# Kernel tuning notes

Hardware: AMD Instinct MI355X
Metric: run time of the kernel (lower is better)

## Reference

```python
import jax, jax.numpy as jnp
import numpy as np

N = 100000      # nodes
E = 1600000     # edges (avg degree 16)
F_IN = 10       # float features; x also carries 2 int index columns
H = 128         # hidden_dim
G = 1000        # graphs
GAP = 3         # gap_len
NPG = N // G    # nodes per graph


def _lin(k, i, o):
    # xavier-uniform-ish init
    lim = np.sqrt(6.0 / (i + o)).astype(np.float32)
    return jax.random.uniform(k, (i, o), jnp.float32, -lim, lim)


def setup_inputs() -> dict:
    key = jax.random.key(0)
    ks = jax.random.split(key, 32)
    xf = jax.random.normal(ks[0], (N, F_IN), jnp.float32)
    ship = jax.random.randint(ks[1], (N, 1), 0, 10).astype(jnp.float32)
    nav = jax.random.randint(ks[2], (N, 1), 0, 10).astype(jnp.float32)
    x = jnp.concatenate([xf, ship, nav], axis=1)  # [N, F_IN+2]
    edge_index = jax.random.randint(ks[3], (2, E), 0, N)
    batch = jnp.arange(N, dtype=jnp.int32) // NPG  # sorted graph ids
    d_in = F_IN + 8  # strip 2 idx cols, add two 4-dim embeddings
    inp = dict(
        x=x, edge_index=edge_index, batch=batch,
        ship_emb=jax.random.normal(ks[4], (10, 4), jnp.float32),
        nav_emb=jax.random.normal(ks[5], (10, 4), jnp.float32),
        W1=_lin(ks[6], d_in, H), b1=jnp.zeros((H,), jnp.float32),
        W2=_lin(ks[7], H, H), b2=jnp.zeros((H,), jnp.float32),
        W3=_lin(ks[8], H, H), b3=jnp.zeros((H,), jnp.float32),
        # GRU params, stored pre-transposed: x @ Wih, gate order (r,z,n)
        Wih_f=_lin(ks[9], H, 3 * H), Whh_f=_lin(ks[10], H, 3 * H),
        bih_f=jnp.zeros((3 * H,), jnp.float32), bhh_f=jnp.zeros((3 * H,), jnp.float32),
        Wih_b=_lin(ks[11], H, 3 * H), Whh_b=_lin(ks[12], H, 3 * H),
        bih_b=jnp.zeros((3 * H,), jnp.float32), bhh_b=jnp.zeros((3 * H,), jnp.float32),
        Wred=_lin(ks[13], 2 * H, H), bred=jnp.zeros((H,), jnp.float32),
        Wh1=_lin(ks[14], 2 * H, H), bh1=jnp.zeros((H,), jnp.float32),
        Wh2=_lin(ks[15], H, 2), bh2=jnp.zeros((2,), jnp.float32),
        num_graphs=G, gap_start_idx=4,
    )
    return inp


def _gru_cell(x, h, Wih, Whh, bih, bhh):
    gi = x @ Wih + bih
    gh = h @ Whh + bhh
    ir, iz, in_ = jnp.split(gi, 3, axis=-1)
    hr, hz, hn = jnp.split(gh, 3, axis=-1)
    r = jax.nn.sigmoid(ir + hr)
    z = jax.nn.sigmoid(iz + hz)
    n = jnp.tanh(in_ + r * hn)
    return (1.0 - z) * n + z * h


def reference(x, edge_index, batch, ship_emb, nav_emb,
              W1, b1, W2, b2, W3, b3,
              Wih_f, Whh_f, bih_f, bhh_f, Wih_b, Whh_b, bih_b, bhh_b,
              Wred, bred, Wh1, bh1, Wh2, bh2, num_graphs, gap_start_idx):
    n_nodes = x.shape[0]
    st = x[:, -2].astype(jnp.int32)
    nv = x[:, -1].astype(jnp.int32)
    feats = jnp.concatenate([x[:, :-2], ship_emb[st], nav_emb[nv]], axis=1)

    src, dst = edge_index[0], edge_index[1]
    # GCN symmetric norm with self-loops: deg over targets + 1
    deg = jax.ops.segment_sum(jnp.ones_like(dst, jnp.float32), dst, num_segments=n_nodes) + 1.0
    dis = jax.lax.rsqrt(deg)  # deg^{-1/2}
    norm = (dis[src] * dis[dst])[:, None]
    self_norm = (dis * dis)[:, None]

    def gcn(h, W, b):
        m = h @ W  # [N,H]
        agg = jax.ops.segment_sum(m[src] * norm, dst, num_segments=n_nodes)
        return agg + m * self_norm + b

    # dropout is eval-mode identity
    h = jax.nn.relu(gcn(feats, W1, b1))
    h = jax.nn.relu(gcn(h, W2, b2))
    h = jax.nn.relu(gcn(h, W3, b3))

    # per-graph gap node = graph offset + gap_start_idx
    counts = jax.ops.segment_sum(jnp.ones_like(batch, jnp.float32), batch, num_segments=num_graphs)
    offsets = jnp.concatenate([jnp.zeros((1,), jnp.float32), jnp.cumsum(counts)[:-1]]).astype(jnp.int32)
    h0 = h[offsets + gap_start_idx]  # [G,H]

    inp, hf, hb = h0, h0, h0
    preds = []
    for _ in range(GAP):
        hf = _gru_cell(inp, hf, Wih_f, Whh_f, bih_f, bhh_f)
        hb = _gru_cell(inp, hb, Wih_b, Whh_b, bih_b, bhh_b)
        out = jnp.concatenate([hf, hb], axis=-1)  # [G,2H]
        preds.append(jax.nn.relu(out @ Wh1 + bh1) @ Wh2 + bh2)
        inp = out @ Wred + bred
    return jnp.stack(preds, axis=1)  # [G, gap_len, 2]
```

## Files before the change

### kernel.cpp

```cpp
#include <hip/hip_runtime.h>
#include <math.h>

#define H 128
#define GAPLEN 3
#define DIN 18

static inline int ceil_div(int a, int b){ return (a + b - 1) / b; }

__device__ __forceinline__ unsigned int bf16pk2(float a, float b){
  unsigned int ua = __float_as_uint(a);
  ua = (ua + 0x7fffu + ((ua >> 16) & 1u)) >> 16;
  unsigned int ub = __float_as_uint(b);
  ub = (ub + 0x7fffu + ((ub >> 16) & 1u)) >> 16;
  return ua | (ub << 16);
}
__device__ __forceinline__ float bf16lo(unsigned int u){ return __uint_as_float(u << 16); }
__device__ __forceinline__ float bf16hi(unsigned int u){ return __uint_as_float(u & 0xffff0000u); }

#define CHUNK 4096

__global__ __launch_bounds__(256) void bhistA_k(const int* __restrict__ ei, int* __restrict__ bh,
                                                int E, int NB){
  __shared__ int lh[1024];
  int t = threadIdx.x;
  for (int j = t; j < 1024; j += 256) lh[j] = 0;
  __syncthreads();
  int base = blockIdx.x * CHUNK;
#pragma unroll
  for (int i = 0; i < 16; ++i){
    int e = base + i * 256 + t;
    if (e < E) atomicAdd(&lh[ei[E + e] >> 7], 1);
  }
  __syncthreads();
  for (int j = t; j < NB; j += 256){
    int v = lh[j];
    if (v) atomicAdd(&bh[j], v);
  }
}

__global__ void bscan_k(const int* __restrict__ bh, int* __restrict__ bbase, int NB){
  __shared__ int sd[1024];
  int t = threadIdx.x;
  int v = (t < NB) ? bh[t] : 0;
  sd[t] = v;
  __syncthreads();
  for (int off = 1; off < 1024; off <<= 1){
    int add = (t >= off) ? sd[t - off] : 0;
    __syncthreads();
    sd[t] += add;
    __syncthreads();
  }
  if (t < NB) bbase[t] = sd[t] - v;
}

__global__ __launch_bounds__(256) void bpartC_k(const int* __restrict__ ei,
                                                const int* __restrict__ bbase,
                                                int* __restrict__ bcur,
                                                int* __restrict__ ebuf, int E, int NB){
  __shared__ int lh[1024];
  __shared__ int lchunk[1024];
  __shared__ int lcur[1024];
  int t = threadIdx.x;
  for (int j = t; j < 1024; j += 256) lh[j] = 0;
  __syncthreads();
  int base = blockIdx.x * CHUNK;
  int pk[16], bk[16];
#pragma unroll
  for (int i = 0; i < 16; ++i){
    int e = base + i * 256 + t;
    if (e < E){
      int s = ei[e];
      int d = ei[E + e];
      bk[i] = d >> 7;
      pk[i] = ((d & 127) << 17) | s;
      atomicAdd(&lh[bk[i]], 1);
    } else bk[i] = -1;
  }
  __syncthreads();
  for (int j = t; j < NB; j += 256){
    int c = lh[j];
    if (c) lchunk[j] = bbase[j] + atomicAdd(&bcur[j], c);
    lcur[j] = 0;
  }
  __syncthreads();
#pragma unroll
  for (int i = 0; i < 16; ++i){
    if (bk[i] >= 0){
      int off = atomicAdd(&lcur[bk[i]], 1);
      ebuf[lchunk[bk[i]] + off] = pk[i];
    }
  }
}

__global__ __launch_bounds__(256) void bbuildD_k(const int* __restrict__ ebuf,
                                                 const int* __restrict__ bh,
                                                 const int* __restrict__ bbase,
                                                 int* __restrict__ rp, int* __restrict__ cnt,
                                                 float* __restrict__ dis, int* __restrict__ csr,
                                                 int n){
  __shared__ int hist[128], sc[128], gb[128], curr[128];
  int b = blockIdx.x;
  int t = threadIdx.x;
  int sb = bbase[b];
  int mb = bh[b];
  if (t < 128) hist[t] = 0;
  __syncthreads();
  for (int i = t; i < mb; i += 256)
    atomicAdd(&hist[ebuf[sb + i] >> 17], 1);
  __syncthreads();
  if (t < 128) sc[t] = hist[t];
  __syncthreads();
  for (int off = 1; off < 128; off <<= 1){
    int add = (t < 128 && t >= off) ? sc[t - off] : 0;
    __syncthreads();
    if (t < 128) sc[t] += add;
    __syncthreads();
  }
  if (t < 128){
    int node = b * 128 + t;
    int rpv = sb + sc[t] - hist[t];
    gb[t] = rpv;
    curr[t] = 0;
    if (node < n){
      rp[node] = rpv;
      cnt[node] = hist[t];
      dis[node] = rsqrtf((float)hist[t] + 1.0f);
    }
  }
  __syncthreads();
  for (int i = t; i < mb; i += 256){
    int p = ebuf[sb + i];
    int dl = p >> 17;
    int src = p & 0x1FFFF;
    int off = atomicAdd(&curr[dl], 1);
    csr[gb[dl] + off] = src;
  }
}

__global__ void dhist_k(const int* __restrict__ cnt, int* __restrict__ dh, int n){
  __shared__ int lh[256];
  int t = threadIdx.x;
  lh[t] = 0;
  __syncthreads();
  int i = blockIdx.x * 256 + t;
  if (i < n){
    int d = cnt[i]; if (d > 255) d = 255;
    atomicAdd(&lh[d], 1);
  }
  __syncthreads();
  if (lh[t]) atomicAdd(&dh[t], lh[t]);
}

__global__ void dscan_k(const int* __restrict__ dh, int* __restrict__ dbase){
  __shared__ int sd[256];
  int t = threadIdx.x;
  int v = dh[t];
  sd[t] = v;
  __syncthreads();
  for (int off = 1; off < 256; off <<= 1){
    int add = (t >= off) ? sd[t - off] : 0;
    __syncthreads();
    sd[t] += add;
    __syncthreads();
  }
  dbase[t] = sd[t] - v;
}

__global__ void dperm_k(const int* __restrict__ cnt, const int* __restrict__ rp,
                        const float* __restrict__ dis, const int* __restrict__ dbase,
                        int* __restrict__ dcur, int4* __restrict__ prc, int n){
  __shared__ int lh[256], lbase[256], lcur[256];
  int t = threadIdx.x;
  lh[t] = 0;
  __syncthreads();
  int i = blockIdx.x * 256 + t;
  bool ok = i < n;
  int d = 0, db = 0;
  if (ok){
    d = cnt[i]; db = d > 255 ? 255 : d;
    atomicAdd(&lh[db], 1);
  }
  __syncthreads();
  int c = lh[t];
  lcur[t] = 0;
  if (c) lbase[t] = dbase[t] + atomicAdd(&dcur[t], c);
  __syncthreads();
  if (ok){
    int off = atomicAdd(&lcur[db], 1);
    int pos = lbase[db] + off;
    prc[pos] = int4{rp[i], d, i, __float_as_int(dis[i])};
  }
}

__global__ void build_feats_k(const float* __restrict__ x, const float* __restrict__ se,
                              const float* __restrict__ ne, const float* __restrict__ dis,
                              unsigned int* __restrict__ f16, int n){
  int i = blockIdx.x * 256 + threadIdx.x;
  if (i >= n) return;
  const float* xr = x + (size_t)i * 12;
  float di = dis[i];
  float v[18];
#pragma unroll
  for (int c = 0; c < 10; ++c) v[c] = di * xr[c];
  int st = (int)xr[10];
  int nv = (int)xr[11];
#pragma unroll
  for (int c = 0; c < 4; ++c){
    v[10 + c] = di * se[st * 4 + c];
    v[14 + c] = di * ne[nv * 4 + c];
  }
  unsigned int* fr = f16 + (size_t)i * 9;
#pragma unroll
  for (int q = 0; q < 9; ++q) fr[q] = bf16pk2(v[2*q], v[2*q + 1]);
}

__global__ __launch_bounds__(256) void agg18b_k(const unsigned int* __restrict__ fw16,
                                                const int4* __restrict__ prc,
                                                const int* __restrict__ csr,
                                                float* __restrict__ out, int n){
  int i = blockIdx.x * 16 + (threadIdx.x >> 4);
  if (i >= n) return;
  int4 v = prc[i];
  int start = v.x, m = v.y, node = v.z;
  float di = __int_as_float(v.w);
  int lane = threadIdx.x & 15;
  bool act = lane < 9;
  float ax = 0.f, ay = 0.f, bx = 0.f, by = 0.f;
  int e = 0;
  for (; e + 4 <= m; e += 4){
    int s0 = csr[start + e + 0];
    int s1 = csr[start + e + 1];
    int s2 = csr[start + e + 2];
    int s3 = csr[start + e + 3];
    if (act){
      unsigned int u0 = fw16[(size_t)s0 * 9 + lane];
      unsigned int u1 = fw16[(size_t)s1 * 9 + lane];
      unsigned int u2 = fw16[(size_t)s2 * 9 + lane];
      unsigned int u3 = fw16[(size_t)s3 * 9 + lane];
      ax += bf16lo(u0) + bf16lo(u1);  ay += bf16hi(u0) + bf16hi(u1);
      bx += bf16lo(u2) + bf16lo(u3);  by += bf16hi(u2) + bf16hi(u3);
    }
  }
  for (; e < m; ++e){
    int s = csr[start + e];
    if (act){
      unsigned int u = fw16[(size_t)s * 9 + lane];
      ax += bf16lo(u); ay += bf16hi(u);
    }
  }
  if (act){
    unsigned int su = fw16[(size_t)node * 9 + lane];
    float2 o;
    o.x = di * (ax + bx + bf16lo(su));
    o.y = di * (ay + by + bf16hi(su));
    *(float2*)&out[(size_t)node * DIN + lane * 2] = o;
  }
}

__global__ __launch_bounds__(256) void agg128b_k(const unsigned int* __restrict__ hw16,
                                                 const int4* __restrict__ prc,
                                                 const int* __restrict__ csr,
                                                 float* __restrict__ out, int n){
  int i = blockIdx.x * 4 + (threadIdx.x >> 6);
  if (i >= n) return;
  int4 v = prc[i];
  int start = __builtin_amdgcn_readfirstlane(v.x);
  int m     = __builtin_amdgcn_readfirstlane(v.y);
  int node  = __builtin_amdgcn_readfirstlane(v.z);
  float di  = __int_as_float(__builtin_amdgcn_readfirstlane(v.w));
  int l = threadIdx.x & 63;
  const unsigned int* hp = hw16 + l;
  float ax0 = 0.f, ay0 = 0.f, ax1 = 0.f, ay1 = 0.f;
  float ax2 = 0.f, ay2 = 0.f, ax3 = 0.f, ay3 = 0.f;
  int e = 0;
  for (; e + 8 <= m; e += 8){
    int s0 = csr[start + e + 0];
    int s1 = csr[start + e + 1];
    int s2 = csr[start + e + 2];
    int s3 = csr[start + e + 3];
    int s4 = csr[start + e + 4];
    int s5 = csr[start + e + 5];
    int s6 = csr[start + e + 6];
    int s7 = csr[start + e + 7];
    unsigned int u0 = hp[(size_t)s0 << 6];
    unsigned int u1 = hp[(size_t)s1 << 6];
    unsigned int u2 = hp[(size_t)s2 << 6];
    unsigned int u3 = hp[(size_t)s3 << 6];
    unsigned int u4 = hp[(size_t)s4 << 6];
    unsigned int u5 = hp[(size_t)s5 << 6];
    unsigned int u6 = hp[(size_t)s6 << 6];
    unsigned int u7 = hp[(size_t)s7 << 6];
    ax0 += bf16lo(u0) + bf16lo(u1);  ay0 += bf16hi(u0) + bf16hi(u1);
    ax1 += bf16lo(u2) + bf16lo(u3);  ay1 += bf16hi(u2) + bf16hi(u3);
    ax2 += bf16lo(u4) + bf16lo(u5);  ay2 += bf16hi(u4) + bf16hi(u5);
    ax3 += bf16lo(u6) + bf16lo(u7);  ay3 += bf16hi(u6) + bf16hi(u7);
  }
  for (; e < m; ++e){
    int s = csr[start + e];
    unsigned int u = hp[(size_t)s << 6];
    ax0 += bf16lo(u); ay0 += bf16hi(u);
  }
  unsigned int su = hp[(size_t)node << 6];
  float2 o;
  o.x = di * (ax0 + ax1 + ax2 + ax3 + bf16lo(su));
  o.y = di * (ay0 + ay1 + ay2 + ay3 + bf16hi(su));
  ((float2*)out)[(size_t)node * 64 + l] = o;
}

__global__ void gemm18_k(const float* __restrict__ A, const float* __restrict__ W,
                         const float* __restrict__ b, const float* __restrict__ dis,
                         unsigned int* __restrict__ C16, int n){
  __shared__ float sw[DIN * H];
  __shared__ float sb[H];
  __shared__ float sa[8][DIN];
  int t = threadIdx.x;
  for (int i = t; i < DIN * H; i += 256) sw[i] = W[i];
  if (t < H) sb[t] = b[t];
  int row0 = blockIdx.x * 8;
  for (int i = t; i < 8 * DIN; i += 256){
    int r = i / DIN, c = i % DIN;
    int rr = row0 + r;
    sa[r][c] = (rr < n) ? A[(size_t)rr * DIN + c] : 0.f;
  }
  __syncthreads();
  int r = t >> 5, lane = t & 31;
  int row = row0 + r;
  if (row >= n) return;
  int c0 = lane * 4;
  float ox = sb[c0], oy = sb[c0 + 1], oz = sb[c0 + 2], ow = sb[c0 + 3];
#pragma unroll
  for (int k = 0; k < DIN; ++k){
    float a = sa[r][k];
    const float4 w = *(const float4*)&sw[k * H + c0];
    ox += a * w.x; oy += a * w.y; oz += a * w.z; ow += a * w.w;
  }
  float di = dis[row];
  uint2 pk;
  pk.x = bf16pk2(di * fmaxf(ox, 0.f), di * fmaxf(oy, 0.f));
  pk.y = bf16pk2(di * fmaxf(oz, 0.f), di * fmaxf(ow, 0.f));
  *(uint2*)&C16[(size_t)row * 64 + lane * 2] = pk;
}

template<int OUTMODE>
__global__ __launch_bounds__(128) void gemm128_k(const float* __restrict__ A,
                                                 const float* __restrict__ B,
                                                 const float* __restrict__ bias,
                                                 const float* __restrict__ dis,
                                                 float* __restrict__ C,
                                                 unsigned int* __restrict__ C16, int n){
  __shared__ float sa[32][64];
  int t = threadIdx.x;
  int row0 = blockIdx.x * 64;
  int tc = t & 15;
  int tr = t >> 4;
  float acc[8][8];
#pragma unroll
  for (int i = 0; i < 8; ++i)
#pragma unroll
    for (int j = 0; j < 8; ++j) acc[i][j] = 0.f;

  int lr = t >> 1;
  int lc = (t & 1) * 16;
  for (int k0 = 0; k0 < H; k0 += 32){
    const float* Ar = A + (size_t)(row0 + lr) * H + k0 + lc;
    bool rowok = (row0 + lr) < n;
    float4 v0, v1, v2, v3;
    if (rowok){
      v0 = *(const float4*)(Ar + 0);
      v1 = *(const float4*)(Ar + 4);
      v2 = *(const float4*)(Ar + 8);
      v3 = *(const float4*)(Ar + 12);
    } else {
      v0 = v1 = v2 = v3 = float4{0.f, 0.f, 0.f, 0.f};
    }
    __syncthreads();
    float vv[16] = {v0.x, v0.y, v0.z, v0.w, v1.x, v1.y, v1.z, v1.w,
                    v2.x, v2.y, v2.z, v2.w, v3.x, v3.y, v3.z, v3.w};
#pragma unroll
    for (int i = 0; i < 16; ++i) sa[lc + i][lr] = vv[i];
    __syncthreads();

    const float* Bp = B + (size_t)k0 * H + tc * 8;
#pragma unroll
    for (int k = 0; k < 32; ++k){
      float4 b0 = *(const float4*)(Bp + (size_t)k * H);
      float4 b1 = *(const float4*)(Bp + (size_t)k * H + 4);
      float4 a0 = *(const float4*)&sa[k][tr * 8];
      float4 a1 = *(const float4*)&sa[k][tr * 8 + 4];
      float aa[8] = {a0.x, a0.y, a0.z, a0.w, a1.x, a1.y, a1.z, a1.w};
      float bb[8] = {b0.x, b0.y, b0.z, b0.w, b1.x, b1.y, b1.z, b1.w};
#pragma unroll
      for (int i = 0; i < 8; ++i)
#pragma unroll
        for (int j = 0; j < 8; ++j) acc[i][j] += aa[i] * bb[j];
    }
  }
  float bb[8];
#pragma unroll
  for (int j = 0; j < 8; ++j) bb[j] = bias[tc * 8 + j];
#pragma unroll
  for (int i = 0; i < 8; ++i){
    int row = row0 + tr * 8 + i;
    if (row < n){
      float o0 = fmaxf(acc[i][0] + bb[0], 0.f);
      float o1 = fmaxf(acc[i][1] + bb[1], 0.f);
      float o2 = fmaxf(acc[i][2] + bb[2], 0.f);
      float o3 = fmaxf(acc[i][3] + bb[3], 0.f);
      float o4 = fmaxf(acc[i][4] + bb[4], 0.f);
      float o5 = fmaxf(acc[i][5] + bb[5], 0.f);
      float o6 = fmaxf(acc[i][6] + bb[6], 0.f);
      float o7 = fmaxf(acc[i][7] + bb[7], 0.f);
      if (OUTMODE == 0){
        float di = dis[row];
        uint4 pk;
        pk.x = bf16pk2(di * o0, di * o1);
        pk.y = bf16pk2(di * o2, di * o3);
        pk.z = bf16pk2(di * o4, di * o5);
        pk.w = bf16pk2(di * o6, di * o7);
        *(uint4*)&C16[(size_t)row * 64 + tc * 4] = pk;
      } else {
        float* Cp = C + (size_t)row * H + tc * 8;
        *(float4*)(Cp)     = float4{o0, o1, o2, o3};
        *(float4*)(Cp + 4) = float4{o4, o5, o6, o7};
      }
    }
  }
}

__global__ void ghist_k(const int* __restrict__ batch, int* __restrict__ gc, int n){
  int i = blockIdx.x * 256 + threadIdx.x;
  if (i < n) atomicAdd(&gc[batch[i]], 1);
}

__global__ void gscan_k(const int* __restrict__ gc, int* __restrict__ go, int G){
  __shared__ int sd[1024];
  int t = threadIdx.x;
  int v = (t < G) ? gc[t] : 0;
  sd[t] = v;
  __syncthreads();
  for (int off = 1; off < 1024; off <<= 1){
    int add = (t >= off) ? sd[t - off] : 0;
    __syncthreads();
    sd[t] += add;
    __syncthreads();
  }
  if (t < G) go[t] = sd[t] - v;
}

__global__ void gather_k(const float* __restrict__ h3, const int* __restrict__ go,
                         const int* __restrict__ gap,
                         float* __restrict__ inp, float* __restrict__ hf,
                         float* __restrict__ hb, int G){
  int g = blockIdx.x;
  int t = threadIdx.x;
  if (g >= G) return;
  int idx = go[g] + gap[0];
  float v = h3[(size_t)idx * H + t];
  inp[(size_t)g * H + t] = v;
  hf[(size_t)g * H + t] = v;
  hb[(size_t)g * H + t] = v;
}

#define GPB 4
__device__ __forceinline__ float sigf(float x){ return 1.f / (1.f + expf(-x)); }

__global__ __launch_bounds__(256) void gru_step_k(
    const float* __restrict__ inp, float* __restrict__ hf, float* __restrict__ hb,
    const float* __restrict__ Wih_f, const float* __restrict__ Whh_f,
    const float* __restrict__ bih_f, const float* __restrict__ bhh_f,
    const float* __restrict__ Wih_b, const float* __restrict__ Whh_b,
    const float* __restrict__ bih_b, const float* __restrict__ bhh_b, int G){
  int cell = blockIdx.y;
  const float* Wih = cell ? Wih_b : Wih_f;
  const float* Whh = cell ? Whh_b : Whh_f;
  const float* bih = cell ? bih_b : bih_f;
  const float* bhh = cell ? bhh_b : bhh_f;
  float* h = cell ? hb : hf;

  __shared__ float sx[GPB][H];
  __shared__ float sh[GPB][H];
  int g0 = blockIdx.x * GPB;
  int t = threadIdx.x;
  for (int i = t; i < GPB * H; i += 256){
    int g = i >> 7, c = i & 127;
    int gg = g0 + g;
    sx[g][c] = (gg < G) ? inp[(size_t)gg * H + c] : 0.f;
    sh[g][c] = (gg < G) ? h[(size_t)gg * H + c] : 0.f;
  }
  __syncthreads();
  int j = t & 127;
  int gs = (t >> 7) * 2;
  float ir[2] = {0,0}, iz[2] = {0,0}, in_[2] = {0,0};
  float hr[2] = {0,0}, hz[2] = {0,0}, hn[2] = {0,0};
#pragma unroll 4
  for (int k = 0; k < H; ++k){
    const float* wi = Wih + (size_t)k * 384;
    const float* wh = Whh + (size_t)k * 384;
    float wr = wi[j], wz = wi[128 + j], wn = wi[256 + j];
    float ur = wh[j], uz = wh[128 + j], un = wh[256 + j];
#pragma unroll
    for (int g = 0; g < 2; ++g){
      float xv = sx[gs + g][k];
      float hv = sh[gs + g][k];
      ir[g] += xv * wr; iz[g] += xv * wz; in_[g] += xv * wn;
      hr[g] += hv * ur; hz[g] += hv * uz; hn[g] += hv * un;
    }
  }
  float bir = bih[j], biz = bih[128 + j], bin = bih[256 + j];
  float bhr = bhh[j], bhz = bhh[128 + j], bhn = bhh[256 + j];
#pragma unroll
  for (int g = 0; g < 2; ++g){
    int gg = g0 + gs + g;
    if (gg < G){
      float r = sigf(ir[g] + bir + hr[g] + bhr);
      float z = sigf(iz[g] + biz + hz[g] + bhz);
      float nn = tanhf(in_[g] + bin + r * (hn[g] + bhn));
      float hv = sh[gs + g][j];
      h[(size_t)gg * H + j] = (1.f - z) * nn + z * hv;
    }
  }
}

__global__ __launch_bounds__(256) void post_step_k(
    const float* __restrict__ hf, const float* __restrict__ hb,
    const float* __restrict__ Wred, const float* __restrict__ bred,
    const float* __restrict__ Wh1, const float* __restrict__ bh1,
    const float* __restrict__ Wh2, const float* __restrict__ bh2,
    float* __restrict__ inp, float* __restrict__ out, int G, int tstep){
  __shared__ float so[GPB][256];
  __shared__ float st1[GPB][H];
  int g0 = blockIdx.x * GPB;
  int t = threadIdx.x;
  for (int i = t; i < GPB * H; i += 256){
    int g = i >> 7, c = i & 127;
    int gg = g0 + g;
    so[g][c]       = (gg < G) ? hf[(size_t)gg * H + c] : 0.f;
    so[g][128 + c] = (gg < G) ? hb[(size_t)gg * H + c] : 0.f;
  }
  __syncthreads();
  int j = t & 127;
  int gs = (t >> 7) * 2;
  float a1[2] = {0,0}, a2[2] = {0,0};
#pragma unroll 8
  for (int k = 0; k < 256; ++k){
    float w1 = Wh1[(size_t)k * H + j];
    float w2 = Wred[(size_t)k * H + j];
#pragma unroll
    for (int g = 0; g < 2; ++g){
      float o = so[gs + g][k];
      a1[g] += o * w1;
      a2[g] += o * w2;
    }
  }
  float B1 = bh1[j], BR = bred[j];
#pragma unroll
  for (int g = 0; g < 2; ++g){
    int gg = g0 + gs + g;
    float t1 = fmaxf(a1[g] + B1, 0.f);
    st1[gs + g][j] = (gg < G) ? t1 : 0.f;
    if (gg < G) inp[(size_t)gg * H + j] = a2[g] + BR;
  }
  __syncthreads();
  if (t < GPB * 2){
    int g = t >> 1, o = t & 1;
    int gg = g0 + g;
    if (gg < G){
      float s = bh2[o];
#pragma unroll 8
      for (int k = 0; k < H; ++k) s += st1[g][k] * Wh2[k * 2 + o];
      out[((size_t)gg * GAPLEN + tstep) * 2 + o] = s;
    }
  }
}

extern "C" void kernel_launch(void* const* d_in, const int* in_sizes, int n_in,
                              void* d_out, int out_size, void* d_ws, size_t ws_size,
                              hipStream_t stream) {
  const float* x     = (const float*)d_in[0];
  const int*   ei    = (const int*)d_in[1];
  const int*   batch = (const int*)d_in[2];
  const float* semb  = (const float*)d_in[3];
  const float* nemb  = (const float*)d_in[4];
  const float* W1 = (const float*)d_in[5];  const float* b1 = (const float*)d_in[6];
  const float* W2 = (const float*)d_in[7];  const float* b2 = (const float*)d_in[8];
  const float* W3 = (const float*)d_in[9];  const float* b3 = (const float*)d_in[10];
  const float* Wih_f = (const float*)d_in[11]; const float* Whh_f = (const float*)d_in[12];
  const float* bih_f = (const float*)d_in[13]; const float* bhh_f = (const float*)d_in[14];
  const float* Wih_b = (const float*)d_in[15]; const float* Whh_b = (const float*)d_in[16];
  const float* bih_b = (const float*)d_in[17]; const float* bhh_b = (const float*)d_in[18];
  const float* Wred = (const float*)d_in[19]; const float* bred = (const float*)d_in[20];
  const float* Wh1  = (const float*)d_in[21]; const float* bh1  = (const float*)d_in[22];
  const float* Wh2  = (const float*)d_in[23]; const float* bh2  = (const float*)d_in[24];
  const int* gap = (const int*)d_in[26];

  int N = in_sizes[0] / 12;
  int E = in_sizes[1] / 2;
  int G = out_size / (GAPLEN * 2);
  int NB = ceil_div(N, 128);
  float* out = (float*)d_out;

  char* ws = (char*)d_ws;
  size_t off = 0;
  auto alloc = [&](size_t bytes) -> void* {
    void* p = ws + off;
    off += (bytes + 511) & ~(size_t)511;
    return p;
  };
  unsigned int* feats16 = (unsigned int*)alloc((size_t)N * 9 * 4);
  float* agg1   = (float*)alloc((size_t)N * DIN * 4);
  float* bufA   = (float*)alloc((size_t)N * H * 4);
  float* bufB   = (float*)alloc((size_t)N * H * 4);
  unsigned int* hb16 = (unsigned int*)alloc((size_t)N * H * 2);
  int*   cnt    = (int*)alloc((size_t)N * 4);
  float* dis    = (float*)alloc((size_t)N * 4);
  int*   rp     = (int*)alloc((size_t)N * 4);
  int*   csr    = (int*)alloc((size_t)E * 4);
  int*   ebuf   = (int*)alloc((size_t)E * 4);
  int4*  prc    = (int4*)alloc((size_t)N * 16);
  int*   bh     = (int*)alloc((size_t)NB * 4);
  int*   bbase  = (int*)alloc((size_t)NB * 4);
  int*   bcur   = (int*)alloc((size_t)NB * 4);
  int*   dh     = (int*)alloc(256 * 4);
  int*   dbase  = (int*)alloc(256 * 4);
  int*   dcur   = (int*)alloc(256 * 4);
  int*   gc     = (int*)alloc((size_t)G * 4);
  int*   go     = (int*)alloc((size_t)G * 4);
  float* ginp   = (float*)alloc((size_t)G * H * 4);
  float* ghf    = (float*)alloc((size_t)G * H * 4);
  float* ghb    = (float*)alloc((size_t)G * H * 4);
  (void)ws_size; (void)n_in;

  hipMemsetAsync(bh, 0, (size_t)NB * 4, stream);
  hipMemsetAsync(bcur, 0, (size_t)NB * 4, stream);
  hipMemsetAsync(dh, 0, 256 * 4, stream);
  hipMemsetAsync(dcur, 0, 256 * 4, stream);
  hipMemsetAsync(gc, 0, (size_t)G * 4, stream);

  int nb256 = ceil_div(N, 256);
  int ebC   = ceil_div(E, CHUNK);

  bhistA_k<<<ebC, 256, 0, stream>>>(ei, bh, E, NB);
  bscan_k<<<1, 1024, 0, stream>>>(bh, bbase, NB);
  bpartC_k<<<ebC, 256, 0, stream>>>(ei, bbase, bcur, ebuf, E, NB);
  bbuildD_k<<<NB, 256, 0, stream>>>(ebuf, bh, bbase, rp, cnt, dis, csr, N);
  dhist_k<<<nb256, 256, 0, stream>>>(cnt, dh, N);
  dscan_k<<<1, 256, 0, stream>>>(dh, dbase);
  dperm_k<<<nb256, 256, 0, stream>>>(cnt, rp, dis, dbase, dcur, prc, N);
  build_feats_k<<<nb256, 256, 0, stream>>>(x, semb, nemb, dis, feats16, N);

  int gemmb = ceil_div(N, 64);

  agg18b_k<<<ceil_div(N, 16), 256, 0, stream>>>(feats16, prc, csr, agg1, N);
  gemm18_k<<<ceil_div(N, 8), 256, 0, stream>>>(agg1, W1, b1, dis, hb16, N);
  agg128b_k<<<ceil_div(N, 4), 256, 0, stream>>>(hb16, prc, csr, bufB, N);
  gemm128_k<0><<<gemmb, 128, 0, stream>>>(bufB, W2, b2, dis, nullptr, hb16, N);
  agg128b_k<<<ceil_div(N, 4), 256, 0, stream>>>(hb16, prc, csr, bufB, N);
  gemm128_k<1><<<gemmb, 128, 0, stream>>>(bufB, W3, b3, dis, bufA, nullptr, N);

  ghist_k<<<nb256, 256, 0, stream>>>(batch, gc, N);
  gscan_k<<<1, 1024, 0, stream>>>(gc, go, G);
  gather_k<<<G, H, 0, stream>>>(bufA, go, gap, ginp, ghf, ghb, G);

  int gb = ceil_div(G, GPB);
  for (int t = 0; t < GAPLEN; ++t){
    gru_step_k<<<dim3(gb, 2), 256, 0, stream>>>(ginp, ghf, ghb,
                                                Wih_f, Whh_f, bih_f, bhh_f,
                                                Wih_b, Whh_b, bih_b, bhh_b, G);
    post_step_k<<<gb, 256, 0, stream>>>(ghf, ghb, Wred, bred, Wh1, bh1, Wh2, bh2,
                                        ginp, out, G, t);
  }
}
```

Baseline: 528.7 us.

## Use split-bf16 MFMA for the 128x128 GCN GEMMs

```diff
diff --git a/kernel.cpp b/kernel.cpp
--- a/kernel.cpp
+++ b/kernel.cpp
@@ -6,6 +6,9 @@
 #define DIN 18
 
 static inline int ceil_div(int a, int b){ return (a + b - 1) / b; }
+
+typedef __attribute__((ext_vector_type(8))) short short8;
+typedef __attribute__((ext_vector_type(4))) float f32x4;
 
 __device__ __forceinline__ unsigned int bf16pk2(float a, float b){
   unsigned int ua = __float_as_uint(a);
@@ -14,6 +17,12 @@
   ub = (ub + 0x7fffu + ((ub >> 16) & 1u)) >> 16;
   return ua | (ub << 16);
 }
+__device__ __forceinline__ unsigned short bf16r(float x){
+  unsigned int u = __float_as_uint(x);
+  u = (u + 0x7fffu + ((u >> 16) & 1u)) >> 16;
+  return (unsigned short)u;
+}
+__device__ __forceinline__ float bfu2f(unsigned short h){ return __uint_as_float((unsigned int)h << 16); }
 __device__ __forceinline__ float bf16lo(unsigned int u){ return __uint_as_float(u << 16); }
 __device__ __forceinline__ float bf16hi(unsigned int u){ return __uint_as_float(u & 0xffff0000u); }
 
@@ -260,7 +269,8 @@
 __global__ __launch_bounds__(256) void agg128b_k(const unsigned int* __restrict__ hw16,
                                                  const int4* __restrict__ prc,
                                                  const int* __restrict__ csr,
-                                                 float* __restrict__ out, int n){
+                                                 unsigned int* __restrict__ Ahi,
+                                                 unsigned int* __restrict__ Alo, int n){
   int i = blockIdx.x * 4 + (threadIdx.x >> 6);
   if (i >= n) return;
   int4 v = prc[i];
@@ -301,10 +311,23 @@
     ax0 += bf16lo(u); ay0 += bf16hi(u);
   }
   unsigned int su = hp[(size_t)node << 6];
-  float2 o;
-  o.x = di * (ax0 + ax1 + ax2 + ax3 + bf16lo(su));
-  o.y = di * (ay0 + ay1 + ay2 + ay3 + bf16hi(su));
-  ((float2*)out)[(size_t)node * 64 + l] = o;
+  float vx = di * (ax0 + ax1 + ax2 + ax3 + bf16lo(su));
+  float vy = di * (ay0 + ay1 + ay2 + ay3 + bf16hi(su));
+  unsigned short hx = bf16r(vx), hy = bf16r(vy);
+  float rx = vx - bfu2f(hx), ry = vy - bfu2f(hy);
+  Ahi[(size_t)node * 64 + l] = (unsigned int)hx | ((unsigned int)hy << 16);
+  Alo[(size_t)node * 64 + l] = (unsigned int)bf16r(rx) | ((unsigned int)bf16r(ry) << 16);
+}
+
+__global__ void wcvt_k(const float* __restrict__ W, unsigned short* __restrict__ hi,
+                       unsigned short* __restrict__ lo){
+  int idx = blockIdx.x * 256 + threadIdx.x;
+  int k = idx >> 7, c = idx & 127;
+  float v = W[idx];
+  unsigned short h = bf16r(v);
+  float r = v - bfu2f(h);
+  hi[(size_t)c * 128 + k] = h;
+  lo[(size_t)c * 128 + k] = bf16r(r);
 }
 
 __global__ void gemm18_k(const float* __restrict__ A, const float* __restrict__ W,
@@ -342,86 +365,64 @@
 }
 
 template<int OUTMODE>
-__global__ __launch_bounds__(128) void gemm128_k(const float* __restrict__ A,
-                                                 const float* __restrict__ B,
-                                                 const float* __restrict__ bias,
-                                                 const float* __restrict__ dis,
-                                                 float* __restrict__ C,
-                                                 unsigned int* __restrict__ C16, int n){
-  __shared__ float sa[32][64];
-  int t = threadIdx.x;
-  int row0 = blockIdx.x * 64;
-  int tc = t & 15;
-  int tr = t >> 4;
-  float acc[8][8];
-#pragma unroll
-  for (int i = 0; i < 8; ++i)
-#pragma unroll
-    for (int j = 0; j < 8; ++j) acc[i][j] = 0.f;
-
-  int lr = t >> 1;
-  int lc = (t & 1) * 16;
-  for (int k0 = 0; k0 < H; k0 += 32){
-    const float* Ar = A + (size_t)(row0 + lr) * H + k0 + lc;
-    bool rowok = (row0 + lr) < n;
-    float4 v0, v1, v2, v3;
-    if (rowok){
-      v0 = *(const float4*)(Ar + 0);
-      v1 = *(const float4*)(Ar + 4);
-      v2 = *(const float4*)(Ar + 8);
-      v3 = *(const float4*)(Ar + 12);
-    } else {
-      v0 = v1 = v2 = v3 = float4{0.f, 0.f, 0.f, 0.f};
-    }
-    __syncthreads();
-    float vv[16] = {v0.x, v0.y, v0.z, v0.w, v1.x, v1.y, v1.z, v1.w,
-                    v2.x, v2.y, v2.z, v2.w, v3.x, v3.y, v3.z, v3.w};
-#pragma unroll
-    for (int i = 0; i < 16; ++i) sa[lc + i][lr] = vv[i];
-    __syncthreads();
-
-    const float* Bp = B + (size_t)k0 * H + tc * 8;
-#pragma unroll
-    for (int k = 0; k < 32; ++k){
-      float4 b0 = *(const float4*)(Bp + (size_t)k * H);
-      float4 b1 = *(const float4*)(Bp + (size_t)k * H + 4);
-      float4 a0 = *(const float4*)&sa[k][tr * 8];
-      float4 a1 = *(const float4*)&sa[k][tr * 8 + 4];
-      float aa[8] = {a0.x, a0.y, a0.z, a0.w, a1.x, a1.y, a1.z, a1.w};
-      float bb[8] = {b0.x, b0.y, b0.z, b0.w, b1.x, b1.y, b1.z, b1.w};
-#pragma unroll
-      for (int i = 0; i < 8; ++i)
-#pragma unroll
-        for (int j = 0; j < 8; ++j) acc[i][j] += aa[i] * bb[j];
-    }
-  }
-  float bb[8];
-#pragma unroll
-  for (int j = 0; j < 8; ++j) bb[j] = bias[tc * 8 + j];
-#pragma unroll
-  for (int i = 0; i < 8; ++i){
-    int row = row0 + tr * 8 + i;
-    if (row < n){
-      float o0 = fmaxf(acc[i][0] + bb[0], 0.f);
-      float o1 = fmaxf(acc[i][1] + bb[1], 0.f);
-      float o2 = fmaxf(acc[i][2] + bb[2], 0.f);
-      float o3 = fmaxf(acc[i][3] + bb[3], 0.f);
-      float o4 = fmaxf(acc[i][4] + bb[4], 0.f);
-      float o5 = fmaxf(acc[i][5] + bb[5], 0.f);
-      float o6 = fmaxf(acc[i][6] + bb[6], 0.f);
-      float o7 = fmaxf(acc[i][7] + bb[7], 0.f);
-      if (OUTMODE == 0){
+__global__ __launch_bounds__(256) void gemm128m_k(const unsigned int* __restrict__ Ahi,
+                                                  const unsigned int* __restrict__ Alo,
+                                                  const unsigned short* __restrict__ BThi,
+                                                  const unsigned short* __restrict__ BTlo,
+                                                  const float* __restrict__ bias,
+                                                  const float* __restrict__ dis,
+                                                  float* __restrict__ C,
+                                                  unsigned short* __restrict__ C16, int n){
+  int t = threadIdx.x;
+  int wid = t >> 6, l = t & 63;
+  int r = l & 15, g = l >> 4;
+  int row0 = blockIdx.x * 128 + wid * 32;
+  f32x4 acc[2][8];
+#pragma unroll
+  for (int rt = 0; rt < 2; ++rt)
+#pragma unroll
+    for (int ct = 0; ct < 8; ++ct) acc[rt][ct] = f32x4{0.f, 0.f, 0.f, 0.f};
+
+#pragma unroll
+  for (int ks = 0; ks < 4; ++ks){
+    short8 ah[2], al[2];
+#pragma unroll
+    for (int rt = 0; rt < 2; ++rt){
+      int row = row0 + rt * 16 + r;
+      if (row >= n) row = n - 1;
+      ah[rt] = *(const short8*)(Ahi + (size_t)row * 64 + ks * 16 + 4 * g);
+      al[rt] = *(const short8*)(Alo + (size_t)row * 64 + ks * 16 + 4 * g);
+    }
+#pragma unroll
+    for (int ct = 0; ct < 8; ++ct){
+      int c = ct * 16 + r;
+      short8 bh = *(const short8*)(BThi + (size_t)c * 128 + ks * 32 + 8 * g);
+      short8 bl = *(const short8*)(BTlo + (size_t)c * 128 + ks * 32 + 8 * g);
+#pragma unroll
+      for (int rt = 0; rt < 2; ++rt){
+        acc[rt][ct] = __builtin_amdgcn_mfma_f32_16x16x32_bf16(ah[rt], bh, acc[rt][ct], 0, 0, 0);
+        acc[rt][ct] = __builtin_amdgcn_mfma_f32_16x16x32_bf16(al[rt], bh, acc[rt][ct], 0, 0, 0);
+        acc[rt][ct] = __builtin_amdgcn_mfma_f32_16x16x32_bf16(ah[rt], bl, acc[rt][ct], 0, 0, 0);
+      }
+    }
+  }
+  float bs[8];
+#pragma unroll
+  for (int ct = 0; ct < 8; ++ct) bs[ct] = bias[ct * 16 + r];
+#pragma unroll
+  for (int rt = 0; rt < 2; ++rt){
+#pragma unroll
+    for (int j = 0; j < 4; ++j){
+      int row = row0 + rt * 16 + 4 * g + j;
+      if (row < n){
         float di = dis[row];
-        uint4 pk;
-        pk.x = bf16pk2(di * o0, di * o1);
-        pk.y = bf16pk2(di * o2, di * o3);
-        pk.z = bf16pk2(di * o4, di * o5);
-        pk.w = bf16pk2(di * o6, di * o7);
-        *(uint4*)&C16[(size_t)row * 64 + tc * 4] = pk;
-      } else {
-        float* Cp = C + (size_t)row * H + tc * 8;
-        *(float4*)(Cp)     = float4{o0, o1, o2, o3};
-        *(float4*)(Cp + 4) = float4{o4, o5, o6, o7};
+#pragma unroll
+        for (int ct = 0; ct < 8; ++ct){
+          int col = ct * 16 + r;
+          float o = fmaxf(acc[rt][ct][j] + bs[ct], 0.f);
+          if (OUTMODE == 0) C16[(size_t)row * 128 + col] = bf16r(di * o);
+          else              C[(size_t)row * 128 + col] = o;
+        }
       }
     }
   }
@@ -609,8 +610,13 @@
   unsigned int* feats16 = (unsigned int*)alloc((size_t)N * 9 * 4);
   float* agg1   = (float*)alloc((size_t)N * DIN * 4);
   float* bufA   = (float*)alloc((size_t)N * H * 4);
-  float* bufB   = (float*)alloc((size_t)N * H * 4);
+  unsigned int* Ahi = (unsigned int*)alloc((size_t)N * 64 * 4);
+  unsigned int* Alo = (unsigned int*)alloc((size_t)N * 64 * 4);
   unsigned int* hb16 = (unsigned int*)alloc((size_t)N * H * 2);
+  unsigned short* w2thi = (unsigned short*)alloc(16384 * 2);
+  unsigned short* w2tlo = (unsigned short*)alloc(16384 * 2);
+  unsigned short* w3thi = (unsigned short*)alloc(16384 * 2);
+  unsigned short* w3tlo = (unsigned short*)alloc(16384 * 2);
   int*   cnt    = (int*)alloc((size_t)N * 4);
   float* dis    = (float*)alloc((size_t)N * 4);
   int*   rp     = (int*)alloc((size_t)N * 4);
@@ -639,6 +645,9 @@
   int nb256 = ceil_div(N, 256);
   int ebC   = ceil_div(E, CHUNK);
 
+  wcvt_k<<<64, 256, 0, stream>>>(W2, w2thi, w2tlo);
+  wcvt_k<<<64, 256, 0, stream>>>(W3, w3thi, w3tlo);
+
   bhistA_k<<<ebC, 256, 0, stream>>>(ei, bh, E, NB);
   bscan_k<<<1, 1024, 0, stream>>>(bh, bbase, NB);
   bpartC_k<<<ebC, 256, 0, stream>>>(ei, bbase, bcur, ebuf, E, NB);
@@ -648,14 +657,16 @@
   dperm_k<<<nb256, 256, 0, stream>>>(cnt, rp, dis, dbase, dcur, prc, N);
   build_feats_k<<<nb256, 256, 0, stream>>>(x, semb, nemb, dis, feats16, N);
 
-  int gemmb = ceil_div(N, 64);
+  int gemmb = ceil_div(N, 128);
 
   agg18b_k<<<ceil_div(N, 16), 256, 0, stream>>>(feats16, prc, csr, agg1, N);
   gemm18_k<<<ceil_div(N, 8), 256, 0, stream>>>(agg1, W1, b1, dis, hb16, N);
-  agg128b_k<<<ceil_div(N, 4), 256, 0, stream>>>(hb16, prc, csr, bufB, N);
-  gemm128_k<0><<<gemmb, 128, 0, stream>>>(bufB, W2, b2, dis, nullptr, hb16, N);
-  agg128b_k<<<ceil_div(N, 4), 256, 0, stream>>>(hb16, prc, csr, bufB, N);
-  gemm128_k<1><<<gemmb, 128, 0, stream>>>(bufB, W3, b3, dis, bufA, nullptr, N);
+  agg128b_k<<<ceil_div(N, 4), 256, 0, stream>>>(hb16, prc, csr, Ahi, Alo, N);
+  gemm128m_k<0><<<gemmb, 256, 0, stream>>>(Ahi, Alo, w2thi, w2tlo, b2, dis,
+                                           nullptr, (unsigned short*)hb16, N);
+  agg128b_k<<<ceil_div(N, 4), 256, 0, stream>>>(hb16, prc, csr, Ahi, Alo, N);
+  gemm128m_k<1><<<gemmb, 256, 0, stream>>>(Ahi, Alo, w3thi, w3tlo, b3, dis,
+                                           bufA, nullptr, N);
 
   ghist_k<<<nb256, 256, 0, stream>>>(batch, gc, N);
   gscan_k<<<1, 1024, 0, stream>>>(gc, go, G);
```

Result: faster. 506.2 us, median of 2 (-4.3%).
